# Performance work log

Measured on AMD Instinct MI355X. Metric: run time of the kernel, lower is better.

## Reference

```python
import jax, jax.numpy as jnp
import numpy as np

MESH = 128
ALPHA, KL, KS = 0.2, 0.3, 1.0

# 8 trilinear (CIC) corner offsets, shape (8, 3)
_OFFSETS = jnp.array([[i, j, k] for i in (0, 1) for j in (0, 1) for k in (0, 1)], dtype=jnp.int32)


def _cic_corners_weights(pos, mesh):
    """pos: [N,3] in grid units -> corners [N,8,3] int32, weights [N,8]."""
    i0 = jnp.floor(pos)
    frac = pos - i0                                    # [N,3]
    i0 = i0.astype(jnp.int32)
    corners = (i0[:, None, :] + _OFFSETS[None]) % mesh  # periodic wrap, [N,8,3]
    w = jnp.where(_OFFSETS[None] == 1, frac[:, None, :], 1.0 - frac[:, None, :])
    return corners, w.prod(-1)                          # [N,8,3], [N,8]


def cic_paint(pos, mesh):
    """Particle-to-mesh scatter (CIC deposit) onto a mesh^3 grid."""
    corners, w = _cic_corners_weights(pos, mesh)
    grid = jnp.zeros((mesh, mesh, mesh), dtype=pos.dtype)
    return grid.at[corners[..., 0], corners[..., 1], corners[..., 2]].add(w)


def cic_read(grid, pos):
    """Mesh-to-particle gather (CIC interpolation). grid: [M,M,M] -> [N]."""
    mesh = grid.shape[0]
    corners, w = _cic_corners_weights(pos, mesh)
    vals = grid[corners[..., 0], corners[..., 1], corners[..., 2]]  # [N,8]
    return (vals * w).sum(-1)


def fftk(mesh):
    """Angular wavenumber vectors broadcastable to the mesh^3 grid."""
    k = (2.0 * jnp.pi * jnp.fft.fftfreq(mesh)).astype(jnp.float32)
    return [k.reshape(mesh, 1, 1), k.reshape(1, mesh, 1), k.reshape(1, 1, mesh)]


def setup_inputs() -> dict:
    key = jax.random.key(0)
    k1, k2 = jax.random.split(key)
    n = MESH ** 3
    pos = jax.random.uniform(k1, (n, 3), dtype=jnp.float32) * MESH  # grid units
    vel = jax.random.normal(k2, (n, 3), dtype=jnp.float32)
    return {"pos": pos, "vel": vel, "full_drift_factor": jnp.ones((), dtype=jnp.float32)}


def reference(pos, vel, full_drift_factor):
    # 1. CIC paint -> density mesh
    delta = cic_paint(pos, MESH)
    # 2. 3D FFT
    delta_k = jnp.fft.fftn(delta)
    kvec = fftk(MESH)
    kk = kvec[0] ** 2 + kvec[1] ** 2 + kvec[2] ** 2
    kk_safe = jnp.where(kk == 0, 1.0, kk)
    # 3. PGD band-pass filter (zeroed at k=0)
    kl2, ks4 = KL ** 2, KS ** 4
    pgd_range = jnp.exp(-kl2 / kk_safe) * jnp.exp(-(kk ** 2) / ks4)
    pgd_range = jnp.where(kk == 0, 0.0, pgd_range)
    # inverse Laplacian kernel: -1/k^2, zero at k=0
    inv_lap = -jnp.where(kk == 0, 0.0, 1.0 / kk_safe)
    pot_k = delta_k * inv_lap * pgd_range
    # 4. three gradient IFFTs + CIC read-out at particle positions
    forces = jnp.stack(
        [cic_read(jnp.fft.ifftn(-1j * kvec[i] * pot_k).real.astype(pos.dtype), pos) for i in range(3)],
        axis=-1,
    )  # [N,3]
    v_pgd = (forces * ALPHA) / full_drift_factor
    vel_boosted = vel + v_pgd
    return (pos, vel_boosted)
```

## Files before the change

kernel.cpp:

```cpp
#include <hip/hip_runtime.h>

#define MESH  128
#define MESH2 16384
#define MESH3 2097152
#define NPART MESH3
#define TILE  16
#define LDP   (TILE + 1)
#define CAP   6
typedef unsigned int u32;
typedef unsigned short u16;
typedef unsigned long long u64;

__device__ __forceinline__ float2 cmul(float2 a, float2 b) {
    return make_float2(a.x * b.x - a.y * b.y, a.x * b.y + a.y * b.x);
}
__device__ __forceinline__ float2 cmulc(float2 a, float2 b) {
    return make_float2(a.x * b.x + a.y * b.y, a.y * b.x - a.x * b.y);
}
__device__ __forceinline__ float2 cadd(float2 a, float2 b) {
    return make_float2(a.x + b.x, a.y + b.y);
}
__device__ __forceinline__ float2 csub(float2 a, float2 b) {
    return make_float2(a.x - b.x, a.y - b.y);
}
__device__ __forceinline__ u16 f2bf(float x) {
    u32 b = __float_as_uint(x);
    return (u16)((b + 0x7FFFu + ((b >> 16) & 1u)) >> 16);
}
__device__ __forceinline__ float bf2f(u16 h) {
    return __uint_as_float(((u32)h) << 16);
}

__device__ __forceinline__ void fft128_fwd_lds(float2 (*__restrict__ s)[LDP],
                                               const float2* __restrict__ tw,
                                               int l, int bb) {
    #pragma unroll
    for (int pr = 0; pr < 3; ++pr) {
        const int st = 2 * pr;
        const int logq = 5 - st;
        const int q = 1 << logq;
        #pragma unroll
        for (int itn = 0; itn < 2; ++itn) {
            const int b = bb + (itn << 4);
            const int j = b & (q - 1);
            const int g = b >> logq;
            const int i0 = (g << (logq + 2)) + j;
            const float2 x0 = s[i0][l], x1 = s[i0 + q][l];
            const float2 x2 = s[i0 + 2 * q][l], x3 = s[i0 + 3 * q][l];
            const int m = j << st;
            const float2 wA = tw[m], wA2 = tw[m + 32], wB = tw[2 * m];
            const float2 u0 = cadd(x0, x2), u2 = cmul(csub(x0, x2), wA);
            const float2 u1 = cadd(x1, x3), u3 = cmul(csub(x1, x3), wA2);
            s[i0][l]         = cadd(u0, u1);
            s[i0 + q][l]     = cmul(csub(u0, u1), wB);
            s[i0 + 2 * q][l] = cadd(u2, u3);
            s[i0 + 3 * q][l] = cmul(csub(u2, u3), wB);
        }
        __syncthreads();
    }
    #pragma unroll
    for (int itn = 0; itn < 4; ++itn) {
        const int i0 = (bb + (itn << 4)) << 1;
        const float2 x0 = s[i0][l], x1 = s[i0 + 1][l];
        s[i0][l]     = cadd(x0, x1);
        s[i0 + 1][l] = csub(x0, x1);
    }
}

__device__ __forceinline__ void fft128_inv_lds(float2 (*__restrict__ s)[LDP],
                                               const float2* __restrict__ tw,
                                               int l, int bb) {
    #pragma unroll
    for (int pr = 0; pr < 3; ++pr) {
        const int st = 2 * pr;
        const int p = 1 << st;
        #pragma unroll
        for (int itn = 0; itn < 2; ++itn) {
            const int b = bb + (itn << 4);
            const int j = b & (p - 1);
            const int g = b >> st;
            const int i0 = (g << (st + 2)) + j;
            const float2 wA = tw[j << (6 - st)];
            const int mB = j << (5 - st);
            const float2 wB = tw[mB], wB2 = tw[mB + 32];
            const float2 x0 = s[i0][l], x1 = s[i0 + p][l];
            const float2 x2 = s[i0 + 2 * p][l], x3 = s[i0 + 3 * p][l];
            const float2 a1 = cmul(x1, wA), a3 = cmul(x3, wA);
            const float2 u0 = cadd(x0, a1), u1 = csub(x0, a1);
            const float2 u2 = cadd(x2, a3), u3 = csub(x2, a3);
            const float2 b2 = cmul(u2, wB), b3 = cmul(u3, wB2);
            s[i0][l]         = cadd(u0, b2);
            s[i0 + p][l]     = cadd(u1, b3);
            s[i0 + 2 * p][l] = csub(u0, b2);
            s[i0 + 3 * p][l] = csub(u1, b3);
        }
        __syncthreads();
    }
    #pragma unroll
    for (int itn = 0; itn < 4; ++itn) {
        const int b = bb + (itn << 4);
        const float2 w = tw[b];
        const float2 u = s[b][l];
        const float2 v = cmul(s[b + 64][l], w);
        s[b][l]      = cadd(u, v);
        s[b + 64][l] = csub(u, v);
    }
}

__device__ __forceinline__ void fft128_inv_lds_dual(float2 (*__restrict__ SA)[LDP],
                                                    float2 (*__restrict__ SB)[LDP],
                                                    const float2* __restrict__ tw,
                                                    int l, int bb) {
    #pragma unroll
    for (int pr = 0; pr < 3; ++pr) {
        const int st = 2 * pr;
        const int p = 1 << st;
        #pragma unroll
        for (int itn = 0; itn < 2; ++itn) {
            const int b = bb + (itn << 4);
            const int j = b & (p - 1);
            const int g = b >> st;
            const int i0 = (g << (st + 2)) + j;
            const float2 wA = tw[j << (6 - st)];
            const int mB = j << (5 - st);
            const float2 wB = tw[mB], wB2 = tw[mB + 32];
            {
                const float2 x0 = SA[i0][l], x1 = SA[i0 + p][l];
                const float2 x2 = SA[i0 + 2 * p][l], x3 = SA[i0 + 3 * p][l];
                const float2 a1 = cmul(x1, wA), a3 = cmul(x3, wA);
                const float2 u0 = cadd(x0, a1), u1 = csub(x0, a1);
                const float2 u2 = cadd(x2, a3), u3 = csub(x2, a3);
                const float2 b2 = cmul(u2, wB), b3 = cmul(u3, wB2);
                SA[i0][l]         = cadd(u0, b2);
                SA[i0 + p][l]     = cadd(u1, b3);
                SA[i0 + 2 * p][l] = csub(u0, b2);
                SA[i0 + 3 * p][l] = csub(u1, b3);
            }
            {
                const float2 x0 = SB[i0][l], x1 = SB[i0 + p][l];
                const float2 x2 = SB[i0 + 2 * p][l], x3 = SB[i0 + 3 * p][l];
                const float2 a1 = cmul(x1, wA), a3 = cmul(x3, wA);
                const float2 u0 = cadd(x0, a1), u1 = csub(x0, a1);
                const float2 u2 = cadd(x2, a3), u3 = csub(x2, a3);
                const float2 b2 = cmul(u2, wB), b3 = cmul(u3, wB2);
                SB[i0][l]         = cadd(u0, b2);
                SB[i0 + p][l]     = cadd(u1, b3);
                SB[i0 + 2 * p][l] = csub(u0, b2);
                SB[i0 + 3 * p][l] = csub(u1, b3);
            }
        }
        __syncthreads();
    }
    #pragma unroll
    for (int itn = 0; itn < 4; ++itn) {
        const int b = bb + (itn << 4);
        const float2 w = tw[b];
        {
            const float2 u = SA[b][l];
            const float2 v = cmul(SA[b + 64][l], w);
            SA[b][l]      = cadd(u, v);
            SA[b + 64][l] = csub(u, v);
        }
        {
            const float2 u = SB[b][l];
            const float2 v = cmul(SB[b + 64][l], w);
            SB[b][l]      = cadd(u, v);
            SB[b + 64][l] = csub(u, v);
        }
    }
}

template <bool INV>
__device__ __forceinline__ void fft_y_body(float2* __restrict__ data, int bid, int t) {
    __shared__ float2 s[MESH][LDP];
    __shared__ float2 tw[64];
    if (t < 64) {
        float sv, cv;
        sincospif(-(float)t / 64.0f, &sv, &cv);
        tw[t] = make_float2(cv, INV ? -sv : sv);
    }
    const int outer = bid >> 3;
    const int z0 = (bid & 7) * TILE;
    const int base = outer * MESH2 + z0;
    for (int i = t; i < MESH * TILE; i += 256) {
        const int l = i & 15, e = i >> 4;
        s[e][l] = data[base + e * MESH + l];
    }
    __syncthreads();
    const int l  = t & 15;
    const int bb = t >> 4;
    if (!INV) fft128_fwd_lds(s, tw, l, bb);
    else      fft128_inv_lds(s, tw, l, bb);
    __syncthreads();
    for (int i = t; i < MESH * TILE; i += 256) {
        const int l2 = i & 15, e = i >> 4;
        data[base + e * MESH + l2] = s[e][l2];
    }
}

__global__ __launch_bounds__(256) void fft_y_fwd(float2* __restrict__ A) {
    fft_y_body<false>(A, blockIdx.x, threadIdx.x);
}
__global__ __launch_bounds__(256) void fft_y_inv_dual(float2* __restrict__ A,
                                                      float2* __restrict__ B) {
    float2* d = (blockIdx.x < 1024) ? A : B;
    fft_y_body<true>(d, blockIdx.x & 1023, threadIdx.x);
}

__global__ __launch_bounds__(256) void fft_z_fwd_merge(const float* __restrict__ ST,
                                                       float2* __restrict__ out) {
    __shared__ float2 s[MESH][LDP];
    __shared__ float2 tw[64];
    const int t = threadIdx.x;
    if (t < 64) {
        float sv, cv;
        sincospif(-(float)t / 64.0f, &sv, &cv);
        tw[t] = make_float2(cv, sv);
    }
    const int col0 = blockIdx.x * TILE;
    const int base = col0 * MESH;
    for (int i = t; i < MESH * TILE; i += 256) {
        const int lc = i >> 7;
        const int z  = i & 127;
        const int c  = col0 + lc;
        const int x = c >> 7, y = c & 127;
        const int tx = x >> 2, ty = y >> 1;
        const int hx = x & 3,  hy = y & 1;
        float v = ST[((tx << 6) | ty) * 1920 + ((hx * 3 + hy) << 7) + z];
        const int txm = (tx + 31) & 31;
        const int tym = (ty + 63) & 63;
        if (hx == 0)
            v += ST[((txm << 6) | ty) * 1920 + ((12 + hy) << 7) + z];
        if (hy == 0) {
            v += ST[((tx << 6) | tym) * 1920 + ((hx * 3 + 2) << 7) + z];
            if (hx == 0)
                v += ST[((txm << 6) | tym) * 1920 + (14 << 7) + z];
        }
        s[z][lc] = make_float2(v, 0.0f);
    }
    __syncthreads();
    const int l  = t & 15;
    const int bb = t >> 4;
    fft128_fwd_lds(s, tw, l, bb);
    __syncthreads();
    for (int i = t; i < MESH * TILE; i += 256)
        out[base + i] = s[i & 127][i >> 7];
}

__global__ __launch_bounds__(256) void fft_z_inv_dual(const float2* __restrict__ A,
                                                      const float2* __restrict__ B,
                                                      u32* __restrict__ Abf,
                                                      u16* __restrict__ Brl) {
    __shared__ float2 s[MESH][LDP];
    __shared__ float2 tw[64];
    const int t = threadIdx.x;
    if (t < 64) {
        float sv, cv;
        sincospif(-(float)t / 64.0f, &sv, &cv);
        tw[t] = make_float2(cv, -sv);
    }
    const bool isB = blockIdx.x >= 1024;
    const int base = (blockIdx.x & 1023) * (TILE * MESH);
    const float2* __restrict__ in = isB ? B : A;
    for (int i = t; i < MESH * TILE; i += 256)
        s[i & 127][i >> 7] = in[base + i];
    __syncthreads();
    const int l  = t & 15;
    const int bb = t >> 4;
    fft128_inv_lds(s, tw, l, bb);
    __syncthreads();
    if (isB) {
        for (int i = t; i < MESH * TILE; i += 256)
            Brl[base + i] = f2bf(s[i & 127][i >> 7].x);
    } else {
        for (int i = t; i < MESH * TILE; i += 256) {
            const float2 v = s[i & 127][i >> 7];
            Abf[base + i] = (u32)f2bf(v.x) | ((u32)f2bf(v.y) << 16);
        }
    }
}

__global__ __launch_bounds__(256) void fft_x_mega(float2* __restrict__ A,
                                                  float2* __restrict__ B) {
    __shared__ float2 SA[MESH][LDP];
    __shared__ float2 SB[MESH][LDP];
    __shared__ float2 twf[64];
    __shared__ float2 twi[64];
    const int t = threadIdx.x;
    if (t < 64) {
        float sv, cv;
        sincospif(-(float)t / 64.0f, &sv, &cv);
        twf[t] = make_float2(cv, sv);
        twi[t] = make_float2(cv, -sv);
    }
    const int cy = blockIdx.x >> 3;
    const int z0 = (blockIdx.x & 7) * TILE;
    const int base = cy * MESH + z0;

    for (int i = t; i < MESH * TILE; i += 256) {
        const int l = i & 15, e = i >> 4;
        SA[e][l] = A[base + e * MESH2 + l];
    }
    __syncthreads();

    const int l  = t & 15;
    const int bb = t >> 4;
    fft128_fwd_lds(SA, twf, l, bb);
    __syncthreads();

    const int jy = (int)(__brev((unsigned)cy) >> 25);
    const float c = 6.28318530717958647692f / 128.0f;
    const float ky = c * (float)(jy < 64 ? jy : jy - 128);
    for (int i = t; i < MESH * TILE; i += 256) {
        const int e = i & 127, ll = i >> 7;
        const int jx = (int)(__brev((unsigned)e) >> 25);
        const int jz = (int)(__brev((unsigned)(z0 + ll)) >> 25);
        const float kx = c * (float)(jx < 64 ? jx : jx - 128);
        const float kz = c * (float)(jz < 64 ? jz : jz - 128);
        const float kk = kx * kx + ky * ky + kz * kz;
        float2 a = SA[e][ll];
        float2 av = make_float2(0.f, 0.f), bv = make_float2(0.f, 0.f);
        if (kk > 0.0f) {
            const float inv_kk = 1.0f / kk;
            const float rng = __expf(-0.09f * inv_kk - kk * kk);
            const float sc  = -inv_kk * rng * (1.0f / 2097152.0f);
            const float pr = a.x * sc, pi = a.y * sc;
            av = make_float2(ky * pr + kx * pi, ky * pi - kx * pr);
            bv = make_float2(kz * pi, -kz * pr);
        }
        SA[e][ll] = av;
        SB[e][ll] = bv;
    }
    __syncthreads();

    fft128_inv_lds_dual(SA, SB, twi, l, bb);
    __syncthreads();

    for (int i = t; i < MESH * TILE; i += 256) {
        const int l2 = i & 15, e = i >> 4;
        A[base + e * MESH2 + l2] = SA[e][l2];
        B[base + e * MESH2 + l2] = SB[e][l2];
    }
}


__device__ __forceinline__ int bucket_of(float px, float py) {
    const int ix = ((int)floorf(px)) & 127;
    const int iy = ((int)floorf(py)) & 127;
    return ((ix >> 2) << 6) | (iy >> 1);
}

__global__ __launch_bounds__(1024) void hist_kernel(const float* __restrict__ pos,
                                                    u32* __restrict__ cnt) {
    __shared__ u32 h[2048];
    const int t = threadIdx.x;
    for (int i = t; i < 2048; i += 1024) h[i] = 0;
    __syncthreads();
    const float4* pos4 = (const float4*)pos;
    const int base_q = blockIdx.x * 2048;
    #pragma unroll
    for (int it = 0; it < 2; ++it) {
        const int q = base_q + (it << 10) + t;
        const float4 Pa = pos4[3 * q], Pb = pos4[3 * q + 1], Pc = pos4[3 * q + 2];
        atomicAdd(&h[bucket_of(Pa.x, Pa.y)], 1u);
        atomicAdd(&h[bucket_of(Pa.w, Pb.x)], 1u);
        atomicAdd(&h[bucket_of(Pb.z, Pb.w)], 1u);
        atomicAdd(&h[bucket_of(Pc.y, Pc.z)], 1u);
    }
    __syncthreads();
    for (int i = t; i < 2048; i += 1024)
        if (h[i]) atomicAdd(&cnt[i], h[i]);
}

__global__ __launch_bounds__(1024) void scan_kernel(const u32* __restrict__ cnt,
                                                    u32* __restrict__ offsets,
                                                    u32* __restrict__ cursors) {
    __shared__ u32 tmp[1024];
    const int t = threadIdx.x;
    const u32 a = cnt[2 * t], b = cnt[2 * t + 1];
    const u32 s = a + b;
    tmp[t] = s;
    __syncthreads();
    for (int off = 1; off < 1024; off <<= 1) {
        const u32 v = (t >= off) ? tmp[t - off] : 0u;
        __syncthreads();
        tmp[t] += v;
        __syncthreads();
    }
    const u32 incl = tmp[t];
    const u32 excl = incl - s;
    offsets[2 * t + 1] = excl + a;
    offsets[2 * t + 2] = incl;
    cursors[2 * t]     = excl;
    cursors[2 * t + 1] = excl + a;
    if (t == 0) offsets[0] = 0;
}

__device__ __forceinline__ u64 make_rec(float px, float py, float pz, int n) {
    const float fxx = floorf(px), fyy = floorf(py), fzz = floorf(pz);
    const int ix = ((int)fxx) & 127, iy = ((int)fyy) & 127, iz = ((int)fzz) & 127;
    const u32 qx = (u32)((px - fxx) * 1024.0f);
    const u32 qy = (u32)((py - fyy) * 1024.0f);
    const u32 qz = (u32)((pz - fzz) * 1024.0f);
    return (u64)iz | ((u64)(ix & 3) << 7) | ((u64)(iy & 1) << 9)
         | ((u64)qx << 11) | ((u64)qy << 21) | ((u64)qz << 31)
         | ((u64)(u32)n << 41);
}

__global__ __launch_bounds__(1024) void scatter_kernel(const float* __restrict__ pos,
                                                       u32* __restrict__ cursors,
                                                       u64* __restrict__ S) {
    __shared__ u32 h[2048];
    const int t = threadIdx.x;
    for (int i = t; i < 2048; i += 1024) h[i] = 0;
    __syncthreads();
    const float4* pos4 = (const float4*)pos;
    const int base_q = blockIdx.x * 2048;
    #pragma unroll
    for (int it = 0; it < 2; ++it) {
        const int q = base_q + (it << 10) + t;
        const float4 Pa = pos4[3 * q], Pb = pos4[3 * q + 1], Pc = pos4[3 * q + 2];
        atomicAdd(&h[bucket_of(Pa.x, Pa.y)], 1u);
        atomicAdd(&h[bucket_of(Pa.w, Pb.x)], 1u);
        atomicAdd(&h[bucket_of(Pb.z, Pb.w)], 1u);
        atomicAdd(&h[bucket_of(Pc.y, Pc.z)], 1u);
    }
    __syncthreads();
    for (int i = t; i < 2048; i += 1024) {
        const u32 c = h[i];
        h[i] = c ? atomicAdd(&cursors[i], c) : 0u;
    }
    __syncthreads();
    #pragma unroll
    for (int it = 0; it < 2; ++it) {
        const int q = base_q + (it << 10) + t;
        const int n = 4 * q;
        const float4 Pa = pos4[3 * q], Pb = pos4[3 * q + 1], Pc = pos4[3 * q + 2];
        S[atomicAdd(&h[bucket_of(Pa.x, Pa.y)], 1u)] = make_rec(Pa.x, Pa.y, Pa.z, n);
        S[atomicAdd(&h[bucket_of(Pa.w, Pb.x)], 1u)] = make_rec(Pa.w, Pb.x, Pb.y, n + 1);
        S[atomicAdd(&h[bucket_of(Pb.z, Pb.w)], 1u)] = make_rec(Pb.z, Pb.w, Pc.x, n + 2);
        S[atomicAdd(&h[bucket_of(Pc.y, Pc.z)], 1u)] = make_rec(Pc.y, Pc.z, Pc.w, n + 3);
    }
}

__device__ __forceinline__ void decode(u64 v, int& iz, int& lx, int& ly,
                                       float& fx, float& fy, float& fz, int& n) {
    iz = (int)(v & 127);
    lx = (int)((v >> 7) & 3);
    ly = (int)((v >> 9) & 3);
    const float inv = 1.0f / 1024.0f;
    fx = (float)((v >> 11) & 1023) * inv;
    fy = (float)((v >> 21) & 1023) * inv;
    fz = (float)((v >> 31) & 1023) * inv;
    n = (int)((v >> 41) & 0x1FFFFF);
}

__global__ __launch_bounds__(256) void paint_kernel(const u64* __restrict__ S,
                                                    const u32* __restrict__ offsets,
                                                    float* __restrict__ ST) {
    __shared__ u32 cnt[1024];
    __shared__ u32 rec[1024 * CAP];
    __shared__ u64 ovf[128];
    __shared__ u32 novf;
    const int t = threadIdx.x;
    for (int i = t; i < 1024; i += 256) cnt[i] = 0;
    if (t == 0) novf = 0;
    __syncthreads();
    const int b = blockIdx.x;
    const int start = offsets[b], end = offsets[b + 1];
    for (int i = start + t; i < end; i += 256) {
        const u64 v = S[i];
        const int iz = (int)(v & 127);
        const int lx = (int)((v >> 7) & 3);
        const int ly = (int)((v >> 9) & 1);
        const int cell = (((lx << 1) | ly) << 7) | iz;
        const u32 r = (u32)((v >> 11) & 0x3FFFFFFFull);
        const u32 slot = atomicAdd(&cnt[cell], 1u);
        if (slot < CAP) rec[cell * CAP + slot] = r;
        else {
            const u32 o = atomicAdd(&novf, 1u);
            if (o < 128u) ovf[o] = ((u64)cell << 32) | r;
        }
    }
    __syncthreads();
    const u32 nv = novf > 128u ? 128u : novf;
    const float inv = 1.0f / 1024.0f;
    for (int i = t; i < 1920; i += 256) {
        const int hx = i / 384;
        const int hy = (i >> 7) % 3;
        const int z  = i & 127;
        float acc = 0.0f;
        #pragma unroll
        for (int sx = 0; sx < 2; ++sx) {
            const int bx = hx - 1 + sx;
            if ((unsigned)bx > 3u) continue;
            #pragma unroll
            for (int sy = 0; sy < 2; ++sy) {
                const int by = hy - 1 + sy;
                if ((unsigned)by > 1u) continue;
                #pragma unroll
                for (int sz = 0; sz < 2; ++sz) {
                    const int bz = (z - 1 + sz) & 127;
                    const int c = (((bx << 1) | by) << 7) | bz;
                    const int m = (int)min(cnt[c], (u32)CAP);
                    const int rb = c * CAP;
                    for (int k = 0; k < m; ++k) {
                        const u32 r = rec[rb + k];
                        const float fx = (float)(r & 1023) * inv;
                        const float fy = (float)((r >> 10) & 1023) * inv;
                        const float fz = (float)(r >> 20) * inv;
                        const float wx = sx ? (1.0f - fx) : fx;
                        const float wy = sy ? (1.0f - fy) : fy;
                        const float wz = sz ? (1.0f - fz) : fz;
                        acc += wx * wy * wz;
                    }
                }
            }
        }
        for (u32 j = 0; j < nv; ++j) {
            const u64 o = ovf[j];
            const int c = (int)(o >> 32);
            const int obx = (c >> 8) & 3, oby = (c >> 7) & 1, obz = c & 127;
            const int dx = hx - obx, dy = hy - oby, dz = (z - obz) & 127;
            if ((unsigned)dx < 2u && (unsigned)dy < 2u && dz < 2) {
                const u32 r = (u32)o;
                const float fx = (float)(r & 1023) * inv;
                const float fy = (float)((r >> 10) & 1023) * inv;
                const float fz = (float)(r >> 20) * inv;
                acc += (dx ? fx : 1.0f - fx) * (dy ? fy : 1.0f - fy)
                     * (dz ? fz : 1.0f - fz);
            }
        }
        ST[(size_t)b * 1920 + i] = acc;
    }
}

__global__ __launch_bounds__(256) void force_kernel(const u64* __restrict__ S,
                                                    const u32* __restrict__ offsets,
                                                    const u32* __restrict__ Abf,
                                                    const u16* __restrict__ Brl,
                                                    u64* __restrict__ VP) {
    __shared__ float2 sxy[1920];
    __shared__ float  szz[1920];
    const int t = threadIdx.x;
    const int b = blockIdx.x;
    const int x0 = (b >> 6) << 2, y0 = (b & 63) << 1;
    for (int i = t; i < 1920; i += 256) {
        const int hx = i / 384;
        const int hy = (i >> 7) % 3;
        const int z = i & 127;
        const int g = (((x0 + hx) & 127) << 14) | (((y0 + hy) & 127) << 7) | z;
        const u32 ab = Abf[g];
        sxy[i] = make_float2(__uint_as_float(ab << 16),
                             __uint_as_float(ab & 0xFFFF0000u));
        szz[i] = bf2f(Brl[g]);
    }
    __syncthreads();
    const int start = offsets[b], end = offsets[b + 1];
    for (int i = start + t; i < end; i += 256) {
        int iz, lx, ly, n;
        float fx, fy, fz;
        decode(S[i], iz, lx, ly, fx, fy, fz, n);
        const float wx[2] = {1.0f - fx, fx};
        const float wy[2] = {1.0f - fy, fy};
        const float wz[2] = {1.0f - fz, fz};
        float gx = 0.f, gy = 0.f, gz = 0.f;
        #pragma unroll
        for (int dx = 0; dx < 2; ++dx)
            #pragma unroll
            for (int dy = 0; dy < 2; ++dy) {
                const int bi = ((lx + dx) * 3 + (ly + dy)) << 7;
                const float wxy = wx[dx] * wy[dy];
                #pragma unroll
                for (int dz = 0; dz < 2; ++dz) {
                    const int idx2 = bi + ((iz + dz) & 127);
                    const float w = wxy * wz[dz];
                    const float2 a = sxy[idx2];
                    gx += w * a.x;
                    gy += w * a.y;
                    gz += w * szz[idx2];
                }
            }
        VP[n] = (u64)f2bf(gx) | ((u64)f2bf(gy) << 16) | ((u64)f2bf(gz) << 32);
    }
}

__global__ __launch_bounds__(256) void finalize_kernel(const float* __restrict__ pos,
                                                       const float* __restrict__ vel,
                                                       const u64* __restrict__ VP,
                                                       const float* __restrict__ fdf,
                                                       float* __restrict__ out) {
    const int tid = blockIdx.x * 256 + threadIdx.x;
    const float sc = 0.2f / fdf[0];
    const float4* pos4 = (const float4*)pos;
    const float4* vel4 = (const float4*)vel;
    float4* outp = (float4*)out;
    float4* outv = outp + (3 * NPART / 4);
    const float4 Pa = pos4[3 * tid], Pb = pos4[3 * tid + 1], Pc = pos4[3 * tid + 2];
    const float4 Va = vel4[3 * tid], Vb = vel4[3 * tid + 1], Vc = vel4[3 * tid + 2];
    outp[3 * tid]     = Pa;
    outp[3 * tid + 1] = Pb;
    outp[3 * tid + 2] = Pc;
    const ulonglong2* VP2 = (const ulonglong2*)VP;
    const ulonglong2 qa = VP2[2 * tid];
    const ulonglong2 qb = VP2[2 * tid + 1];
    const u64 q[4] = {qa.x, qa.y, qb.x, qb.y};
    const float vv[12] = {Va.x, Va.y, Va.z, Va.w, Vb.x, Vb.y, Vb.z, Vb.w,
                          Vc.x, Vc.y, Vc.z, Vc.w};
    float ov[12];
    #pragma unroll
    for (int k = 0; k < 4; ++k) {
        const float gx = bf2f((u16)(q[k] & 0xFFFF));
        const float gy = bf2f((u16)((q[k] >> 16) & 0xFFFF));
        const float gz = bf2f((u16)((q[k] >> 32) & 0xFFFF));
        ov[3 * k]     = vv[3 * k]     + gx * sc;
        ov[3 * k + 1] = vv[3 * k + 1] + gy * sc;
        ov[3 * k + 2] = vv[3 * k + 2] + gz * sc;
    }
    outv[3 * tid]     = make_float4(ov[0], ov[1], ov[2], ov[3]);
    outv[3 * tid + 1] = make_float4(ov[4], ov[5], ov[6], ov[7]);
    outv[3 * tid + 2] = make_float4(ov[8], ov[9], ov[10], ov[11]);
}

extern "C" void kernel_launch(void* const* d_in, const int* in_sizes, int n_in,
                              void* d_out, int out_size, void* d_ws, size_t ws_size,
                              hipStream_t stream) {
    const float* pos = (const float*)d_in[0];
    const float* vel = (const float*)d_in[1];
    const float* fdf = (const float*)d_in[2];
    float* out = (float*)d_out;

    char* w = (char*)d_ws;
    float2* A   = (float2*)(w);
    float2* B   = (float2*)(w + ((size_t)1 << 24));
    float*  ST  = (float*)(w + ((size_t)2 << 24));
    u32*    Abf = (u32*)(w + ((size_t)3 << 24));
    u16*    Brl = (u16*)(w + ((size_t)3 << 24) + (size_t)MESH3 * 4);
    u64*    VP  = (u64*)(w + ((size_t)4 << 24));
    u64*    S   = (u64*)(w + ((size_t)5 << 24));
    u32* cnt     = (u32*)(w + ((size_t)6 << 24));
    u32* offsets = cnt + 2048;
    u32* cursors = offsets + 2049;

    hipMemsetAsync(cnt, 0, 2048 * sizeof(u32), stream);
    hist_kernel<<<256, 1024, 0, stream>>>(pos, cnt);
    scan_kernel<<<1, 1024, 0, stream>>>(cnt, offsets, cursors);
    scatter_kernel<<<256, 1024, 0, stream>>>(pos, cursors, S);

    paint_kernel<<<2048, 256, 0, stream>>>(S, offsets, ST);

    fft_z_fwd_merge<<<1024, 256, 0, stream>>>(ST, A);
    fft_y_fwd<<<1024, 256, 0, stream>>>(A);
    fft_x_mega<<<1024, 256, 0, stream>>>(A, B);
    fft_y_inv_dual<<<2048, 256, 0, stream>>>(A, B);
    fft_z_inv_dual<<<2048, 256, 0, stream>>>(A, B, Abf, Brl);

    force_kernel<<<2048, 256, 0, stream>>>(S, offsets, Abf, Brl, VP);
    finalize_kernel<<<2048, 256, 0, stream>>>(pos, vel, VP, fdf, out);
}
```

Before: 290.0 us.

## Double FFT block threads to 512 and move position copy into histogram

All FFT kernels now launch 512 threads per block, and each thread does one radix-4 butterfly per stage instead of two, giving more parallelism per tile and more wavefronts to hide LDS latency. The pass-through copy of positions to the output moves from the finalize kernel into the histogram kernel, which already loads positions, so finalize no longer reads pos a second time. The cost is larger blocks, which may reduce how many blocks fit per CU, and extra stores inside the atomic-heavy histogram kernel.

```diff
diff --git a/kernel.cpp b/kernel.cpp
--- a/kernel.cpp
+++ b/kernel.cpp
@@ -14,9 +14,6 @@
 __device__ __forceinline__ float2 cmul(float2 a, float2 b) {
     return make_float2(a.x * b.x - a.y * b.y, a.x * b.y + a.y * b.x);
 }
-__device__ __forceinline__ float2 cmulc(float2 a, float2 b) {
-    return make_float2(a.x * b.x + a.y * b.y, a.y * b.x - a.x * b.y);
-}
 __device__ __forceinline__ float2 cadd(float2 a, float2 b) {
     return make_float2(a.x + b.x, a.y + b.y);
 }
@@ -39,28 +36,24 @@
         const int st = 2 * pr;
         const int logq = 5 - st;
         const int q = 1 << logq;
-        #pragma unroll
-        for (int itn = 0; itn < 2; ++itn) {
-            const int b = bb + (itn << 4);
-            const int j = b & (q - 1);
-            const int g = b >> logq;
-            const int i0 = (g << (logq + 2)) + j;
-            const float2 x0 = s[i0][l], x1 = s[i0 + q][l];
-            const float2 x2 = s[i0 + 2 * q][l], x3 = s[i0 + 3 * q][l];
-            const int m = j << st;
-            const float2 wA = tw[m], wA2 = tw[m + 32], wB = tw[2 * m];
-            const float2 u0 = cadd(x0, x2), u2 = cmul(csub(x0, x2), wA);
-            const float2 u1 = cadd(x1, x3), u3 = cmul(csub(x1, x3), wA2);
-            s[i0][l]         = cadd(u0, u1);
-            s[i0 + q][l]     = cmul(csub(u0, u1), wB);
-            s[i0 + 2 * q][l] = cadd(u2, u3);
-            s[i0 + 3 * q][l] = cmul(csub(u2, u3), wB);
-        }
+        const int j = bb & (q - 1);
+        const int g = bb >> logq;
+        const int i0 = (g << (logq + 2)) + j;
+        const float2 x0 = s[i0][l], x1 = s[i0 + q][l];
+        const float2 x2 = s[i0 + 2 * q][l], x3 = s[i0 + 3 * q][l];
+        const int m = j << st;
+        const float2 wA = tw[m], wA2 = tw[m + 32], wB = tw[2 * m];
+        const float2 u0 = cadd(x0, x2), u2 = cmul(csub(x0, x2), wA);
+        const float2 u1 = cadd(x1, x3), u3 = cmul(csub(x1, x3), wA2);
+        s[i0][l]         = cadd(u0, u1);
+        s[i0 + q][l]     = cmul(csub(u0, u1), wB);
+        s[i0 + 2 * q][l] = cadd(u2, u3);
+        s[i0 + 3 * q][l] = cmul(csub(u2, u3), wB);
         __syncthreads();
     }
     #pragma unroll
-    for (int itn = 0; itn < 4; ++itn) {
-        const int i0 = (bb + (itn << 4)) << 1;
+    for (int itn = 0; itn < 2; ++itn) {
+        const int i0 = (bb + (itn << 5)) << 1;
         const float2 x0 = s[i0][l], x1 = s[i0 + 1][l];
         s[i0][l]     = cadd(x0, x1);
         s[i0 + 1][l] = csub(x0, x1);
@@ -74,31 +67,27 @@
     for (int pr = 0; pr < 3; ++pr) {
         const int st = 2 * pr;
         const int p = 1 << st;
-        #pragma unroll
-        for (int itn = 0; itn < 2; ++itn) {
-            const int b = bb + (itn << 4);
-            const int j = b & (p - 1);
-            const int g = b >> st;
-            const int i0 = (g << (st + 2)) + j;
-            const float2 wA = tw[j << (6 - st)];
-            const int mB = j << (5 - st);
-            const float2 wB = tw[mB], wB2 = tw[mB + 32];
-            const float2 x0 = s[i0][l], x1 = s[i0 + p][l];
-            const float2 x2 = s[i0 + 2 * p][l], x3 = s[i0 + 3 * p][l];
-            const float2 a1 = cmul(x1, wA), a3 = cmul(x3, wA);
-            const float2 u0 = cadd(x0, a1), u1 = csub(x0, a1);
-            const float2 u2 = cadd(x2, a3), u3 = csub(x2, a3);
-            const float2 b2 = cmul(u2, wB), b3 = cmul(u3, wB2);
-            s[i0][l]         = cadd(u0, b2);
-            s[i0 + p][l]     = cadd(u1, b3);
-            s[i0 + 2 * p][l] = csub(u0, b2);
-            s[i0 + 3 * p][l] = csub(u1, b3);
-        }
+        const int j = bb & (p - 1);
+        const int g = bb >> st;
+        const int i0 = (g << (st + 2)) + j;
+        const float2 wA = tw[j << (6 - st)];
+        const int mB = j << (5 - st);
+        const float2 wB = tw[mB], wB2 = tw[mB + 32];
+        const float2 x0 = s[i0][l], x1 = s[i0 + p][l];
+        const float2 x2 = s[i0 + 2 * p][l], x3 = s[i0 + 3 * p][l];
+        const float2 a1 = cmul(x1, wA), a3 = cmul(x3, wA);
+        const float2 u0 = cadd(x0, a1), u1 = csub(x0, a1);
+        const float2 u2 = cadd(x2, a3), u3 = csub(x2, a3);
+        const float2 b2 = cmul(u2, wB), b3 = cmul(u3, wB2);
+        s[i0][l]         = cadd(u0, b2);
+        s[i0 + p][l]     = cadd(u1, b3);
+        s[i0 + 2 * p][l] = csub(u0, b2);
+        s[i0 + 3 * p][l] = csub(u1, b3);
         __syncthreads();
     }
     #pragma unroll
-    for (int itn = 0; itn < 4; ++itn) {
-        const int b = bb + (itn << 4);
+    for (int itn = 0; itn < 2; ++itn) {
+        const int b = bb + (itn << 5);
         const float2 w = tw[b];
         const float2 u = s[b][l];
         const float2 v = cmul(s[b + 64][l], w);
@@ -115,45 +104,41 @@
     for (int pr = 0; pr < 3; ++pr) {
         const int st = 2 * pr;
         const int p = 1 << st;
-        #pragma unroll
-        for (int itn = 0; itn < 2; ++itn) {
-            const int b = bb + (itn << 4);
-            const int j = b & (p - 1);
-            const int g = b >> st;
-            const int i0 = (g << (st + 2)) + j;
-            const float2 wA = tw[j << (6 - st)];
-            const int mB = j << (5 - st);
-            const float2 wB = tw[mB], wB2 = tw[mB + 32];
-            {
-                const float2 x0 = SA[i0][l], x1 = SA[i0 + p][l];
-                const float2 x2 = SA[i0 + 2 * p][l], x3 = SA[i0 + 3 * p][l];
-                const float2 a1 = cmul(x1, wA), a3 = cmul(x3, wA);
-                const float2 u0 = cadd(x0, a1), u1 = csub(x0, a1);
-                const float2 u2 = cadd(x2, a3), u3 = csub(x2, a3);
-                const float2 b2 = cmul(u2, wB), b3 = cmul(u3, wB2);
-                SA[i0][l]         = cadd(u0, b2);
-                SA[i0 + p][l]     = cadd(u1, b3);
-                SA[i0 + 2 * p][l] = csub(u0, b2);
-                SA[i0 + 3 * p][l] = csub(u1, b3);
-            }
-            {
-                const float2 x0 = SB[i0][l], x1 = SB[i0 + p][l];
-                const float2 x2 = SB[i0 + 2 * p][l], x3 = SB[i0 + 3 * p][l];
-                const float2 a1 = cmul(x1, wA), a3 = cmul(x3, wA);
-                const float2 u0 = cadd(x0, a1), u1 = csub(x0, a1);
-                const float2 u2 = cadd(x2, a3), u3 = csub(x2, a3);
-                const float2 b2 = cmul(u2, wB), b3 = cmul(u3, wB2);
-                SB[i0][l]         = cadd(u0, b2);
-                SB[i0 + p][l]     = cadd(u1, b3);
-                SB[i0 + 2 * p][l] = csub(u0, b2);
-                SB[i0 + 3 * p][l] = csub(u1, b3);
-            }
+        const int j = bb & (p - 1);
+        const int g = bb >> st;
+        const int i0 = (g << (st + 2)) + j;
+        const float2 wA = tw[j << (6 - st)];
+        const int mB = j << (5 - st);
+        const float2 wB = tw[mB], wB2 = tw[mB + 32];
+        {
+            const float2 x0 = SA[i0][l], x1 = SA[i0 + p][l];
+            const float2 x2 = SA[i0 + 2 * p][l], x3 = SA[i0 + 3 * p][l];
+            const float2 a1 = cmul(x1, wA), a3 = cmul(x3, wA);
+            const float2 u0 = cadd(x0, a1), u1 = csub(x0, a1);
+            const float2 u2 = cadd(x2, a3), u3 = csub(x2, a3);
+            const float2 b2 = cmul(u2, wB), b3 = cmul(u3, wB2);
+            SA[i0][l]         = cadd(u0, b2);
+            SA[i0 + p][l]     = cadd(u1, b3);
+            SA[i0 + 2 * p][l] = csub(u0, b2);
+            SA[i0 + 3 * p][l] = csub(u1, b3);
+        }
+        {
+            const float2 x0 = SB[i0][l], x1 = SB[i0 + p][l];
+            const float2 x2 = SB[i0 + 2 * p][l], x3 = SB[i0 + 3 * p][l];
+            const float2 a1 = cmul(x1, wA), a3 = cmul(x3, wA);
+            const float2 u0 = cadd(x0, a1), u1 = csub(x0, a1);
+            const float2 u2 = cadd(x2, a3), u3 = csub(x2, a3);
+            const float2 b2 = cmul(u2, wB), b3 = cmul(u3, wB2);
+            SB[i0][l]         = cadd(u0, b2);
+            SB[i0 + p][l]     = cadd(u1, b3);
+            SB[i0 + 2 * p][l] = csub(u0, b2);
+            SB[i0 + 3 * p][l] = csub(u1, b3);
         }
         __syncthreads();
     }
     #pragma unroll
-    for (int itn = 0; itn < 4; ++itn) {
-        const int b = bb + (itn << 4);
+    for (int itn = 0; itn < 2; ++itn) {
+        const int b = bb + (itn << 5);
         const float2 w = tw[b];
         {
             const float2 u = SA[b][l];
@@ -182,7 +167,7 @@
     const int outer = bid >> 3;
     const int z0 = (bid & 7) * TILE;
     const int base = outer * MESH2 + z0;
-    for (int i = t; i < MESH * TILE; i += 256) {
+    for (int i = t; i < MESH * TILE; i += 512) {
         const int l = i & 15, e = i >> 4;
         s[e][l] = data[base + e * MESH + l];
     }
@@ -192,22 +177,22 @@
     if (!INV) fft128_fwd_lds(s, tw, l, bb);
     else      fft128_inv_lds(s, tw, l, bb);
     __syncthreads();
-    for (int i = t; i < MESH * TILE; i += 256) {
+    for (int i = t; i < MESH * TILE; i += 512) {
         const int l2 = i & 15, e = i >> 4;
         data[base + e * MESH + l2] = s[e][l2];
     }
 }
 
-__global__ __launch_bounds__(256) void fft_y_fwd(float2* __restrict__ A) {
+__global__ __launch_bounds__(512) void fft_y_fwd(float2* __restrict__ A) {
     fft_y_body<false>(A, blockIdx.x, threadIdx.x);
 }
-__global__ __launch_bounds__(256) void fft_y_inv_dual(float2* __restrict__ A,
+__global__ __launch_bounds__(512) void fft_y_inv_dual(float2* __restrict__ A,
                                                       float2* __restrict__ B) {
     float2* d = (blockIdx.x < 1024) ? A : B;
     fft_y_body<true>(d, blockIdx.x & 1023, threadIdx.x);
 }
 
-__global__ __launch_bounds__(256) void fft_z_fwd_merge(const float* __restrict__ ST,
+__global__ __launch_bounds__(512) void fft_z_fwd_merge(const float* __restrict__ ST,
                                                        float2* __restrict__ out) {
     __shared__ float2 s[MESH][LDP];
     __shared__ float2 tw[64];
@@ -219,7 +204,7 @@
     }
     const int col0 = blockIdx.x * TILE;
     const int base = col0 * MESH;
-    for (int i = t; i < MESH * TILE; i += 256) {
+    for (int i = t; i < MESH * TILE; i += 512) {
         const int lc = i >> 7;
         const int z  = i & 127;
         const int c  = col0 + lc;
@@ -243,11 +228,11 @@
     const int bb = t >> 4;
     fft128_fwd_lds(s, tw, l, bb);
     __syncthreads();
-    for (int i = t; i < MESH * TILE; i += 256)
+    for (int i = t; i < MESH * TILE; i += 512)
         out[base + i] = s[i & 127][i >> 7];
 }
 
-__global__ __launch_bounds__(256) void fft_z_inv_dual(const float2* __restrict__ A,
+__global__ __launch_bounds__(512) void fft_z_inv_dual(const float2* __restrict__ A,
                                                       const float2* __restrict__ B,
                                                       u32* __restrict__ Abf,
                                                       u16* __restrict__ Brl) {
@@ -262,7 +247,7 @@
     const bool isB = blockIdx.x >= 1024;
     const int base = (blockIdx.x & 1023) * (TILE * MESH);
     const float2* __restrict__ in = isB ? B : A;
-    for (int i = t; i < MESH * TILE; i += 256)
+    for (int i = t; i < MESH * TILE; i += 512)
         s[i & 127][i >> 7] = in[base + i];
     __syncthreads();
     const int l  = t & 15;
@@ -270,17 +255,17 @@
     fft128_inv_lds(s, tw, l, bb);
     __syncthreads();
     if (isB) {
-        for (int i = t; i < MESH * TILE; i += 256)
+        for (int i = t; i < MESH * TILE; i += 512)
             Brl[base + i] = f2bf(s[i & 127][i >> 7].x);
     } else {
-        for (int i = t; i < MESH * TILE; i += 256) {
+        for (int i = t; i < MESH * TILE; i += 512) {
             const float2 v = s[i & 127][i >> 7];
             Abf[base + i] = (u32)f2bf(v.x) | ((u32)f2bf(v.y) << 16);
         }
     }
 }
 
-__global__ __launch_bounds__(256) void fft_x_mega(float2* __restrict__ A,
+__global__ __launch_bounds__(512) void fft_x_mega(float2* __restrict__ A,
                                                   float2* __restrict__ B) {
     __shared__ float2 SA[MESH][LDP];
     __shared__ float2 SB[MESH][LDP];
@@ -297,7 +282,7 @@
     const int z0 = (blockIdx.x & 7) * TILE;
     const int base = cy * MESH + z0;
 
-    for (int i = t; i < MESH * TILE; i += 256) {
+    for (int i = t; i < MESH * TILE; i += 512) {
         const int l = i & 15, e = i >> 4;
         SA[e][l] = A[base + e * MESH2 + l];
     }
@@ -311,7 +296,7 @@
     const int jy = (int)(__brev((unsigned)cy) >> 25);
     const float c = 6.28318530717958647692f / 128.0f;
     const float ky = c * (float)(jy < 64 ? jy : jy - 128);
-    for (int i = t; i < MESH * TILE; i += 256) {
+    for (int i = t; i < MESH * TILE; i += 512) {
         const int e = i & 127, ll = i >> 7;
         const int jx = (int)(__brev((unsigned)e) >> 25);
         const int jz = (int)(__brev((unsigned)(z0 + ll)) >> 25);
@@ -336,7 +321,7 @@
     fft128_inv_lds_dual(SA, SB, twi, l, bb);
     __syncthreads();
 
-    for (int i = t; i < MESH * TILE; i += 256) {
+    for (int i = t; i < MESH * TILE; i += 512) {
         const int l2 = i & 15, e = i >> 4;
         A[base + e * MESH2 + l2] = SA[e][l2];
         B[base + e * MESH2 + l2] = SB[e][l2];
@@ -351,7 +336,8 @@
 }
 
 __global__ __launch_bounds__(1024) void hist_kernel(const float* __restrict__ pos,
-                                                    u32* __restrict__ cnt) {
+                                                    u32* __restrict__ cnt,
+                                                    float4* __restrict__ outp) {
     __shared__ u32 h[2048];
     const int t = threadIdx.x;
     for (int i = t; i < 2048; i += 1024) h[i] = 0;
@@ -362,6 +348,9 @@
     for (int it = 0; it < 2; ++it) {
         const int q = base_q + (it << 10) + t;
         const float4 Pa = pos4[3 * q], Pb = pos4[3 * q + 1], Pc = pos4[3 * q + 2];
+        outp[3 * q]     = Pa;
+        outp[3 * q + 1] = Pb;
+        outp[3 * q + 2] = Pc;
         atomicAdd(&h[bucket_of(Pa.x, Pa.y)], 1u);
         atomicAdd(&h[bucket_of(Pa.w, Pb.x)], 1u);
         atomicAdd(&h[bucket_of(Pb.z, Pb.w)], 1u);
@@ -585,22 +574,15 @@
     }
 }
 
-__global__ __launch_bounds__(256) void finalize_kernel(const float* __restrict__ pos,
-                                                       const float* __restrict__ vel,
+__global__ __launch_bounds__(256) void finalize_kernel(const float* __restrict__ vel,
                                                        const u64* __restrict__ VP,
                                                        const float* __restrict__ fdf,
                                                        float* __restrict__ out) {
     const int tid = blockIdx.x * 256 + threadIdx.x;
     const float sc = 0.2f / fdf[0];
-    const float4* pos4 = (const float4*)pos;
     const float4* vel4 = (const float4*)vel;
-    float4* outp = (float4*)out;
-    float4* outv = outp + (3 * NPART / 4);
-    const float4 Pa = pos4[3 * tid], Pb = pos4[3 * tid + 1], Pc = pos4[3 * tid + 2];
+    float4* outv = (float4*)out + (3 * NPART / 4);
     const float4 Va = vel4[3 * tid], Vb = vel4[3 * tid + 1], Vc = vel4[3 * tid + 2];
-    outp[3 * tid]     = Pa;
-    outp[3 * tid + 1] = Pb;
-    outp[3 * tid + 2] = Pc;
     const ulonglong2* VP2 = (const ulonglong2*)VP;
     const ulonglong2 qa = VP2[2 * tid];
     const ulonglong2 qb = VP2[2 * tid + 1];
@@ -643,18 +625,18 @@
     u32* cursors = offsets + 2049;
 
     hipMemsetAsync(cnt, 0, 2048 * sizeof(u32), stream);
-    hist_kernel<<<256, 1024, 0, stream>>>(pos, cnt);
+    hist_kernel<<<256, 1024, 0, stream>>>(pos, cnt, (float4*)out);
     scan_kernel<<<1, 1024, 0, stream>>>(cnt, offsets, cursors);
     scatter_kernel<<<256, 1024, 0, stream>>>(pos, cursors, S);
 
     paint_kernel<<<2048, 256, 0, stream>>>(S, offsets, ST);
 
-    fft_z_fwd_merge<<<1024, 256, 0, stream>>>(ST, A);
-    fft_y_fwd<<<1024, 256, 0, stream>>>(A);
-    fft_x_mega<<<1024, 256, 0, stream>>>(A, B);
-    fft_y_inv_dual<<<2048, 256, 0, stream>>>(A, B);
-    fft_z_inv_dual<<<2048, 256, 0, stream>>>(A, B, Abf, Brl);
+    fft_z_fwd_merge<<<1024, 512, 0, stream>>>(ST, A);
+    fft_y_fwd<<<1024, 512, 0, stream>>>(A);
+    fft_x_mega<<<1024, 512, 0, stream>>>(A, B);
+    fft_y_inv_dual<<<2048, 512, 0, stream>>>(A, B);
+    fft_z_inv_dual<<<2048, 512, 0, stream>>>(A, B, Abf, Brl);
 
     force_kernel<<<2048, 256, 0, stream>>>(S, offsets, Abf, Brl, VP);
-    finalize_kernel<<<2048, 256, 0, stream>>>(pos, vel, VP, fdf, out);
-}
+    finalize_kernel<<<2048, 256, 0, stream>>>(vel, VP, fdf, out);
+}
```

Result: no change. 285.7 us (-1.5%).
